# Optimization experiments

Measured on AMD Instinct MI355X. Metric: run time of the kernel, lower is better.

Reference implementation:

```python
import jax, jax.numpy as jnp
import numpy as np

N_HEADS = 1

def setup_inputs() -> dict:
    key = jax.random.key(0)
    kq, kk, kv = jax.random.split(key, 3)
    B, G, H, S = 16, 32, 32, 4096  # batch, n_var (groups), hidden_dim, seq_len
    q = jax.random.normal(kq, (B, G, H, S), dtype=jnp.float32)
    k = jax.random.normal(kk, (B, G, H, S), dtype=jnp.float32)
    v = jax.random.normal(kv, (B, G, H, S), dtype=jnp.float32)
    return {"q": q, "k": k, "v": v}

def reference(q, k, v):
    # q, k, v: (B, G, hidden_dim, S); n_heads = 1 as used by TAMCaD_T
    B, Gq, hidden, S = q.shape
    Gkv = k.shape[1]
    nh = N_HEADS
    dk = hidden // nh
    scale = dk ** -0.5
    qr = q.reshape(B, Gq, nh, dk, S)
    kr = k.reshape(B, Gkv, nh, dk, S)
    vr = v.reshape(B, Gkv, nh, dk, S)
    # logits: (B, nh, S, Gq, Gkv) -- attention over variable pairs per timestep
    logits = scale * jnp.einsum('bghds,bfhds->bhsgf', qr, kr)
    attn = jax.nn.softmax(logits, axis=-1)
    # x: (B, nh, S, Gq, dk)
    x = jnp.einsum('bhsgf,bfhds->bhsgd', attn, vr)
    # permute (0,3,1,4,2) -> (B, Gq, nh, dk, S) -> (B, Gq*nh*dk, S)
    x = x.transpose(0, 3, 1, 4, 2).reshape(B, Gq * nh * dk, S)
    # attentions/logits: mean over heads, then (B, Gq, Gkv, S)
    attentions = attn.mean(axis=1).transpose(0, 2, 3, 1)
    attention_logits = logits.mean(axis=1).transpose(0, 2, 3, 1)
    return x, attentions, attention_logits
```

## Files before the change

kernel.cpp:

```cpp
#include <hip/hip_runtime.h>
#include <hip/hip_bf16.h>


constexpr int S_LEN = 4096;
constexpr int GG = 32;
constexpr int HH = 32;
constexpr int TS = 16;
constexpr float SCALE = 0.17677669529663687f;

__device__ __forceinline__ unsigned bf16pack(float a, float b) {
    unsigned ua = __float_as_uint(a);
    unsigned ub = __float_as_uint(b);
    ua = (ua + 0x7fffu + ((ua >> 16) & 1u)) >> 16;
    ub = (ub + 0x7fffu + ((ub >> 16) & 1u)) >> 16;
    return ua | (ub << 16);
}

__global__ __launch_bounds__(512, 4) void tamcad_fused(
    const float* __restrict__ q, const float* __restrict__ k,
    const float* __restrict__ v, float* __restrict__ x_out,
    float* __restrict__ attn_out, float* __restrict__ logit_out)
{
    __shared__ __align__(16) unsigned k_lds[GG * HH * TS / 2];
    __shared__ __align__(16) unsigned v_lds[GG * HH * TS / 2];

    const int nwg = gridDim.x;
    const int cpx = nwg >> 3;
    const int raw = blockIdx.x;
    const int logical = (raw & 7) * cpx + (raw >> 3);
    const int b  = logical >> 8;
    const int st = logical & 255;
    const int s0 = st * TS;

    const int tid = threadIdx.x;
    const int gt = tid >> 6;
    const int ft = (tid >> 3) & 7;
    const int sp = tid & 7;

    const int baseB = b * (GG * HH);
    const float* qb = q + (size_t)baseB * S_LEN + s0;
    const float* kb = k + (size_t)baseB * S_LEN + s0;
    const float* vb = v + (size_t)baseB * S_LEN + s0;

    for (int r = tid; r < GG * HH; r += 512) {
        const int f = r >> 5, d = r & 31;
        const float4* ks = reinterpret_cast<const float4*>(kb + (size_t)r * S_LEN);
        const float4* vs = reinterpret_cast<const float4*>(vb + (size_t)r * S_LEN);
        float4 k0 = ks[0], k1 = ks[1], k2 = ks[2], k3 = ks[3];
        float4 v0 = vs[0], v1 = vs[1], v2 = vs[2], v3 = vs[3];
        uint4 kl, kh, vl, vh;
        kl.x = bf16pack(k0.x, k0.y); kl.y = bf16pack(k0.z, k0.w);
        kl.z = bf16pack(k1.x, k1.y); kl.w = bf16pack(k1.z, k1.w);
        kh.x = bf16pack(k2.x, k2.y); kh.y = bf16pack(k2.z, k2.w);
        kh.z = bf16pack(k3.x, k3.y); kh.w = bf16pack(k3.z, k3.w);
        vl.x = bf16pack(v0.x, v0.y); vl.y = bf16pack(v0.z, v0.w);
        vl.z = bf16pack(v1.x, v1.y); vl.w = bf16pack(v1.z, v1.w);
        vh.x = bf16pack(v2.x, v2.y); vh.y = bf16pack(v2.z, v2.w);
        vh.z = bf16pack(v3.x, v3.y); vh.w = bf16pack(v3.z, v3.w);
        const int rk = f * 32 + ((d + (f >> 2)) & 31);
        const int xk = rk & 4;
        *reinterpret_cast<uint4*>(&k_lds[rk * 8 + xk])       = kl;
        *reinterpret_cast<uint4*>(&k_lds[rk * 8 + (4 ^ xk)]) = kh;
        const int rv = f * 32 + (((d & 3) << 3) | (d >> 2));
        const int xv = rv & 4;
        *reinterpret_cast<uint4*>(&v_lds[rv * 8 + xv])       = vl;
        *reinterpret_cast<uint4*>(&v_lds[rv * 8 + (4 ^ xv)]) = vh;
    }
    __syncthreads();

    float acc[4][4][2];
    #pragma unroll
    for (int j = 0; j < 4; ++j)
        #pragma unroll
        for (int i = 0; i < 4; ++i) { acc[j][i][0] = 0.f; acc[j][i][1] = 0.f; }

    const float* qrow[4];
    #pragma unroll
    for (int j = 0; j < 4; ++j)
        qrow[j] = qb + (size_t)((gt * 4 + j) * HH) * S_LEN + sp * 2;

    #pragma unroll 4
    for (int d = 0; d < HH; ++d) {
        float2 qv[4];
        #pragma unroll
        for (int j = 0; j < 4; ++j)
            qv[j] = *reinterpret_cast<const float2*>(qrow[j] + (size_t)d * S_LEN);
        const int dd = (d + ft) & 31;
        const int so = sp ^ (dd & 4);
        #pragma unroll
        for (int i = 0; i < 4; ++i) {
            const unsigned w = k_lds[((ft * 4 + i) * 32 + dd) * 8 + so];
            const float klo = __uint_as_float(w << 16);
            const float khi = __uint_as_float(w & 0xffff0000u);
            #pragma unroll
            for (int j = 0; j < 4; ++j) {
                acc[j][i][0] = fmaf(qv[j].x, klo, acc[j][i][0]);
                acc[j][i][1] = fmaf(qv[j].y, khi, acc[j][i][1]);
            }
        }
    }
    #pragma unroll
    for (int j = 0; j < 4; ++j)
        #pragma unroll
        for (int i = 0; i < 4; ++i) { acc[j][i][0] *= SCALE; acc[j][i][1] *= SCALE; }

    float mx[4][2];
    #pragma unroll
    for (int j = 0; j < 4; ++j) {
        #pragma unroll
        for (int e = 0; e < 2; ++e) {
            float m = fmaxf(fmaxf(acc[j][0][e], acc[j][1][e]),
                            fmaxf(acc[j][2][e], acc[j][3][e]));
            m = fmaxf(m, __shfl_xor(m, 8));
            m = fmaxf(m, __shfl_xor(m, 16));
            m = fmaxf(m, __shfl_xor(m, 32));
            mx[j][e] = m;
        }
    }
    #pragma unroll
    for (int j = 0; j < 4; ++j) {
        const int g = gt * 4 + j;
        #pragma unroll
        for (int i = 0; i < 4; ++i) {
            const int f = ft * 4 + i;
            const size_t o = (size_t)(baseB + g * GG + f) * S_LEN + s0 + sp * 2;
            *reinterpret_cast<float2*>(logit_out + o) = make_float2(acc[j][i][0], acc[j][i][1]);
            acc[j][i][0] = __expf(acc[j][i][0] - mx[j][0]);
            acc[j][i][1] = __expf(acc[j][i][1] - mx[j][1]);
        }
    }
    float inv[4][2];
    #pragma unroll
    for (int j = 0; j < 4; ++j) {
        #pragma unroll
        for (int e = 0; e < 2; ++e) {
            float s = acc[j][0][e] + acc[j][1][e] + acc[j][2][e] + acc[j][3][e];
            s += __shfl_xor(s, 8);
            s += __shfl_xor(s, 16);
            s += __shfl_xor(s, 32);
            inv[j][e] = __builtin_amdgcn_rcpf(s);
        }
    }
    unsigned apack[4][4];
    #pragma unroll
    for (int j = 0; j < 4; ++j) {
        const int g = gt * 4 + j;
        #pragma unroll
        for (int i = 0; i < 4; ++i) {
            const int f = ft * 4 + i;
            const float a0 = acc[j][i][0] * inv[j][0];
            const float a1 = acc[j][i][1] * inv[j][1];
            const size_t o = (size_t)(baseB + g * GG + f) * S_LEN + s0 + sp * 2;
            *reinterpret_cast<float2*>(attn_out + o) = make_float2(a0, a1);
            apack[i][j] = bf16pack(a0, a1);
        }
    }
    __syncthreads();
    #pragma unroll
    for (int i = 0; i < 4; ++i) {
        const int f = ft * 4 + i;
        uint4 w;
        w.x = apack[i][0]; w.y = apack[i][1]; w.z = apack[i][2]; w.w = apack[i][3];
        *reinterpret_cast<uint4*>(&k_lds[((f * 8 + gt) * 8 + (sp ^ ft)) * 4]) = w;
    }
    __syncthreads();

    float xacc[4][4][2];
    #pragma unroll
    for (int j = 0; j < 4; ++j)
        #pragma unroll
        for (int i = 0; i < 4; ++i) { xacc[j][i][0] = 0.f; xacc[j][i][1] = 0.f; }

    const int dt = ft;
    const int sov = sp ^ (dt & 4);
    #pragma unroll 4
    for (int f = 0; f < GG; ++f) {
        const int fp = f >> 2;
        const uint4 wa = *reinterpret_cast<const uint4*>(
            &k_lds[((f * 8 + gt) * 8 + (sp ^ fp)) * 4]);
        float alo[4], ahi[4];
        alo[0] = __uint_as_float(wa.x << 16); ahi[0] = __uint_as_float(wa.x & 0xffff0000u);
        alo[1] = __uint_as_float(wa.y << 16); ahi[1] = __uint_as_float(wa.y & 0xffff0000u);
        alo[2] = __uint_as_float(wa.z << 16); ahi[2] = __uint_as_float(wa.z & 0xffff0000u);
        alo[3] = __uint_as_float(wa.w << 16); ahi[3] = __uint_as_float(wa.w & 0xffff0000u);
        #pragma unroll
        for (int i = 0; i < 4; ++i) {
            const unsigned w = v_lds[(f * 32 + i * 8 + dt) * 8 + sov];
            const float vlo = __uint_as_float(w << 16);
            const float vhi = __uint_as_float(w & 0xffff0000u);
            #pragma unroll
            for (int j = 0; j < 4; ++j) {
                xacc[j][i][0] = fmaf(alo[j], vlo, xacc[j][i][0]);
                xacc[j][i][1] = fmaf(ahi[j], vhi, xacc[j][i][1]);
            }
        }
    }
    #pragma unroll
    for (int j = 0; j < 4; ++j) {
        const int g = gt * 4 + j;
        #pragma unroll
        for (int i = 0; i < 4; ++i) {
            const int d = dt * 4 + i;
            const size_t o = (size_t)(baseB + g * HH + d) * S_LEN + s0 + sp * 2;
            *reinterpret_cast<float2*>(x_out + o) = make_float2(xacc[j][i][0], xacc[j][i][1]);
        }
    }
}

extern "C" void kernel_launch(void* const* d_in, const int* in_sizes, int n_in,
                              void* d_out, int out_size, void* d_ws, size_t ws_size,
                              hipStream_t stream) {
    const float* q = (const float*)d_in[0];
    const float* k = (const float*)d_in[1];
    const float* v = (const float*)d_in[2];
    float* out = (float*)d_out;
    const int n = in_sizes[0];
    const int B = n / (GG * HH * S_LEN);
    float* x_out     = out;
    float* attn_out  = out + (size_t)n;
    float* logit_out = out + (size_t)2 * n;
    const int nwg = B * (S_LEN / TS);
    tamcad_fused<<<dim3(nwg), dim3(512), 0, stream>>>(q, k, v, x_out, attn_out, logit_out);
}
```

Baseline: 513.3 us.

## Read K and V directly from global memory instead of staging in LDS as bf16

Drops the cooperative LDS staging of K and V, which converted them to bf16, and has each thread load K and V float2 values straight from global memory inside the two contraction loops. This removes a block-wide sync and the LDS footprint, which may let more workgroups fit per CU. K is now used at full fp32 precision. Each K/V element is now read by several waves, relying on L1/L2 caching, and the global loads in the inner loops add latency.

Result: slower. 923.6 us (+79.9%).

```diff
diff --git a/kernel.cpp b/kernel.cpp
--- a/kernel.cpp
+++ b/kernel.cpp
@@ -1,5 +1,4 @@
 #include <hip/hip_runtime.h>
-#include <hip/hip_bf16.h>
 
 
 constexpr int S_LEN = 4096;
@@ -21,8 +20,7 @@
     const float* __restrict__ v, float* __restrict__ x_out,
     float* __restrict__ attn_out, float* __restrict__ logit_out)
 {
-    __shared__ __align__(16) unsigned k_lds[GG * HH * TS / 2];
-    __shared__ __align__(16) unsigned v_lds[GG * HH * TS / 2];
+    __shared__ __align__(16) unsigned a_lds[GG * 64 * 4];
 
     const int nwg = gridDim.x;
     const int cpx = nwg >> 3;
@@ -38,35 +36,9 @@
     const int sp = tid & 7;
 
     const int baseB = b * (GG * HH);
-    const float* qb = q + (size_t)baseB * S_LEN + s0;
-    const float* kb = k + (size_t)baseB * S_LEN + s0;
-    const float* vb = v + (size_t)baseB * S_LEN + s0;
-
-    for (int r = tid; r < GG * HH; r += 512) {
-        const int f = r >> 5, d = r & 31;
-        const float4* ks = reinterpret_cast<const float4*>(kb + (size_t)r * S_LEN);
-        const float4* vs = reinterpret_cast<const float4*>(vb + (size_t)r * S_LEN);
-        float4 k0 = ks[0], k1 = ks[1], k2 = ks[2], k3 = ks[3];
-        float4 v0 = vs[0], v1 = vs[1], v2 = vs[2], v3 = vs[3];
-        uint4 kl, kh, vl, vh;
-        kl.x = bf16pack(k0.x, k0.y); kl.y = bf16pack(k0.z, k0.w);
-        kl.z = bf16pack(k1.x, k1.y); kl.w = bf16pack(k1.z, k1.w);
-        kh.x = bf16pack(k2.x, k2.y); kh.y = bf16pack(k2.z, k2.w);
-        kh.z = bf16pack(k3.x, k3.y); kh.w = bf16pack(k3.z, k3.w);
-        vl.x = bf16pack(v0.x, v0.y); vl.y = bf16pack(v0.z, v0.w);
-        vl.z = bf16pack(v1.x, v1.y); vl.w = bf16pack(v1.z, v1.w);
-        vh.x = bf16pack(v2.x, v2.y); vh.y = bf16pack(v2.z, v2.w);
-        vh.z = bf16pack(v3.x, v3.y); vh.w = bf16pack(v3.z, v3.w);
-        const int rk = f * 32 + ((d + (f >> 2)) & 31);
-        const int xk = rk & 4;
-        *reinterpret_cast<uint4*>(&k_lds[rk * 8 + xk])       = kl;
-        *reinterpret_cast<uint4*>(&k_lds[rk * 8 + (4 ^ xk)]) = kh;
-        const int rv = f * 32 + (((d & 3) << 3) | (d >> 2));
-        const int xv = rv & 4;
-        *reinterpret_cast<uint4*>(&v_lds[rv * 8 + xv])       = vl;
-        *reinterpret_cast<uint4*>(&v_lds[rv * 8 + (4 ^ xv)]) = vh;
-    }
-    __syncthreads();
+    const float* qb = q + (size_t)baseB * S_LEN + s0 + sp * 2;
+    const float* kb = k + (size_t)baseB * S_LEN + s0 + sp * 2;
+    const float* vb = v + (size_t)baseB * S_LEN + s0 + sp * 2;
 
     float acc[4][4][2];
     #pragma unroll
@@ -74,29 +46,32 @@
         #pragma unroll
         for (int i = 0; i < 4; ++i) { acc[j][i][0] = 0.f; acc[j][i][1] = 0.f; }
 
-    const float* qrow[4];
-    #pragma unroll
-    for (int j = 0; j < 4; ++j)
-        qrow[j] = qb + (size_t)((gt * 4 + j) * HH) * S_LEN + sp * 2;
-
-    #pragma unroll 4
-    for (int d = 0; d < HH; ++d) {
-        float2 qv[4];
+    {
+        const float* qrow[4];
+        const float* krow[4];
         #pragma unroll
         for (int j = 0; j < 4; ++j)
-            qv[j] = *reinterpret_cast<const float2*>(qrow[j] + (size_t)d * S_LEN);
-        const int dd = (d + ft) & 31;
-        const int so = sp ^ (dd & 4);
-        #pragma unroll
-        for (int i = 0; i < 4; ++i) {
-            const unsigned w = k_lds[((ft * 4 + i) * 32 + dd) * 8 + so];
-            const float klo = __uint_as_float(w << 16);
-            const float khi = __uint_as_float(w & 0xffff0000u);
-            #pragma unroll
-            for (int j = 0; j < 4; ++j) {
-                acc[j][i][0] = fmaf(qv[j].x, klo, acc[j][i][0]);
-                acc[j][i][1] = fmaf(qv[j].y, khi, acc[j][i][1]);
-            }
+            qrow[j] = qb + (size_t)((gt * 4 + j) * HH) * S_LEN;
+        #pragma unroll
+        for (int i = 0; i < 4; ++i)
+            krow[i] = kb + (size_t)((ft * 4 + i) * HH) * S_LEN;
+
+        #pragma unroll 4
+        for (int d = 0; d < HH; ++d) {
+            float2 qv[4], kv[4];
+            #pragma unroll
+            for (int j = 0; j < 4; ++j)
+                qv[j] = *reinterpret_cast<const float2*>(qrow[j] + (size_t)d * S_LEN);
+            #pragma unroll
+            for (int i = 0; i < 4; ++i)
+                kv[i] = *reinterpret_cast<const float2*>(krow[i] + (size_t)d * S_LEN);
+            #pragma unroll
+            for (int i = 0; i < 4; ++i)
+                #pragma unroll
+                for (int j = 0; j < 4; ++j) {
+                    acc[j][i][0] = fmaf(qv[j].x, kv[i].x, acc[j][i][0]);
+                    acc[j][i][1] = fmaf(qv[j].y, kv[i].y, acc[j][i][1]);
+                }
         }
     }
     #pragma unroll
@@ -155,13 +130,12 @@
             apack[i][j] = bf16pack(a0, a1);
         }
     }
-    __syncthreads();
     #pragma unroll
     for (int i = 0; i < 4; ++i) {
         const int f = ft * 4 + i;
         uint4 w;
         w.x = apack[i][0]; w.y = apack[i][1]; w.z = apack[i][2]; w.w = apack[i][3];
-        *reinterpret_cast<uint4*>(&k_lds[((f * 8 + gt) * 8 + (sp ^ ft)) * 4]) = w;
+        *reinterpret_cast<uint4*>(&a_lds[(f * 64 + gt * 8 + (sp ^ ft)) * 4]) = w;
     }
     __syncthreads();
 
@@ -171,36 +145,40 @@
         #pragma unroll
         for (int i = 0; i < 4; ++i) { xacc[j][i][0] = 0.f; xacc[j][i][1] = 0.f; }
 
-    const int dt = ft;
-    const int sov = sp ^ (dt & 4);
-    #pragma unroll 4
-    for (int f = 0; f < GG; ++f) {
-        const int fp = f >> 2;
-        const uint4 wa = *reinterpret_cast<const uint4*>(
-            &k_lds[((f * 8 + gt) * 8 + (sp ^ fp)) * 4]);
-        float alo[4], ahi[4];
-        alo[0] = __uint_as_float(wa.x << 16); ahi[0] = __uint_as_float(wa.x & 0xffff0000u);
-        alo[1] = __uint_as_float(wa.y << 16); ahi[1] = __uint_as_float(wa.y & 0xffff0000u);
-        alo[2] = __uint_as_float(wa.z << 16); ahi[2] = __uint_as_float(wa.z & 0xffff0000u);
-        alo[3] = __uint_as_float(wa.w << 16); ahi[3] = __uint_as_float(wa.w & 0xffff0000u);
+    {
+        const int dt = ft;
+        const float* vrow[4];
+        #pragma unroll
+        for (int i = 0; i < 4; ++i)
+            vrow[i] = vb + (size_t)(dt * 4 + i) * S_LEN;
+
+        #pragma unroll 4
+        for (int f = 0; f < GG; ++f) {
+            const uint4 wa = *reinterpret_cast<const uint4*>(
+                &a_lds[(f * 64 + gt * 8 + (sp ^ (f >> 2))) * 4]);
+            float alo[4], ahi[4];
+            alo[0] = __uint_as_float(wa.x << 16); ahi[0] = __uint_as_float(wa.x & 0xffff0000u);
+            alo[1] = __uint_as_float(wa.y << 16); ahi[1] = __uint_as_float(wa.y & 0xffff0000u);
+            alo[2] = __uint_as_float(wa.z << 16); ahi[2] = __uint_as_float(wa.z & 0xffff0000u);
+            alo[3] = __uint_as_float(wa.w << 16); ahi[3] = __uint_as_float(wa.w & 0xffff0000u);
+            #pragma unroll
+            for (int i = 0; i < 4; ++i) {
+                const float2 vv = *reinterpret_cast<const float2*>(
+                    vrow[i] + (size_t)(f * HH) * S_LEN);
+                #pragma unroll
+                for (int j = 0; j < 4; ++j) {
+                    xacc[j][i][0] = fmaf(alo[j], vv.x, xacc[j][i][0]);
+                    xacc[j][i][1] = fmaf(ahi[j], vv.y, xacc[j][i][1]);
+                }
+            }
+        }
+    }
+    #pragma unroll
+    for (int j = 0; j < 4; ++j) {
+        const int g = gt * 4 + j;
         #pragma unroll
         for (int i = 0; i < 4; ++i) {
-            const unsigned w = v_lds[(f * 32 + i * 8 + dt) * 8 + sov];
-            const float vlo = __uint_as_float(w << 16);
-            const float vhi = __uint_as_float(w & 0xffff0000u);
-            #pragma unroll
-            for (int j = 0; j < 4; ++j) {
-                xacc[j][i][0] = fmaf(alo[j], vlo, xacc[j][i][0]);
-                xacc[j][i][1] = fmaf(ahi[j], vhi, xacc[j][i][1]);
-            }
-        }
-    }
-    #pragma unroll
-    for (int j = 0; j < 4; ++j) {
-        const int g = gt * 4 + j;
-        #pragma unroll
-        for (int i = 0; i < 4; ++i) {
-            const int d = dt * 4 + i;
+            const int d = ft * 4 + i;
             const size_t o = (size_t)(baseB + g * HH + d) * S_LEN + s0 + sp * 2;
             *reinterpret_cast<float2*>(x_out + o) = make_float2(xacc[j][i][0], xacc[j][i][1]);
         }
```
